# Performance work log

Measured on AMD Instinct MI355X. Metric: run time of the kernel, lower is better.

The kernel has to match this reference:

```python
import jax, jax.numpy as jnp
import numpy as np

EPS = 1e-5
S_CENTERS = 1024  # npoint//4
NSAMPLE = 32


def index_points(pts, idx):
    # pts [B,N,C], idx [B,...] int -> [B,...,C]
    return jax.vmap(lambda p, i: p[i])(pts, idx)


def farthest_point_sample(xyz, npoint):
    # xyz [B,N,3] -> [B,npoint] indices (deterministic start at index 0)
    B, N, _ = xyz.shape
    def body(carry, _):
        dist, far = carry
        centroid = jnp.take_along_axis(xyz, far[:, None, None], axis=1)  # [B,1,3]
        d = jnp.sum((xyz - centroid) ** 2, axis=-1)                      # [B,N]
        dist = jnp.minimum(dist, d)
        nxt = jnp.argmax(dist, axis=-1).astype(jnp.int32)
        return (dist, nxt), far
    init = (jnp.full((B, N), 1e10, xyz.dtype), jnp.zeros((B,), jnp.int32))
    _, idx = jax.lax.scan(body, init, None, length=npoint)
    return jnp.transpose(idx)  # [B,npoint]


def knn_point(k, xyz, new_xyz):
    # squared dists [B,S,N], take k nearest
    d = (jnp.sum(new_xyz ** 2, -1)[:, :, None]
         + jnp.sum(xyz ** 2, -1)[:, None, :]
         - 2.0 * jnp.einsum('bsc,bnc->bsn', new_xyz, xyz))
    _, idx = jax.lax.top_k(-d, k)
    return idx  # [B,S,k]


def instance_norm(h):
    # h [B,S,K,C]: InstanceNorm2d (affine=False) normalizes per (b,c) over spatial dims
    mu = jnp.mean(h, axis=(1, 2), keepdims=True)
    var = jnp.var(h, axis=(1, 2), keepdims=True)
    return (h - mu) * jax.lax.rsqrt(var + EPS)


def setup_inputs() -> dict:
    key = jax.random.key(0)
    ks = jax.random.split(key, 12)
    B, N, C = 8, 4096, 128
    inp = {
        'pc1_l_loc2': jax.random.normal(ks[0], (B, 3, N), jnp.float32),
        'corr_feats': jax.random.normal(ks[1], (B, C, N), jnp.float32),
        'W1': jax.random.normal(ks[2], (128, 131), jnp.float32) * 0.05,
        'b1': jnp.zeros((128,), jnp.float32),
        'W2': jax.random.normal(ks[3], (128, 128), jnp.float32) * 0.05,
        'b2': jnp.zeros((128,), jnp.float32),
        'W3': jax.random.normal(ks[4], (128, 128), jnp.float32) * 0.05,
        'b3': jnp.zeros((128,), jnp.float32),
        'fc_w': jax.random.normal(ks[5], (3, 128), jnp.float32) * 0.05,
        'fc_b': jnp.zeros((3,), jnp.float32),
    }
    return inp


def reference(pc1_l_loc2, corr_feats, W1, b1, W2, b2, W3, b3, fc_w, fc_b):
    xyz = jnp.transpose(pc1_l_loc2, (0, 2, 1))    # [B,N,3]
    points = jnp.transpose(corr_feats, (0, 2, 1))  # [B,N,128]

    fps_idx = farthest_point_sample(xyz, S_CENTERS)           # [B,S]
    new_xyz = index_points(xyz, fps_idx)                      # [B,S,3]
    idx = knn_point(NSAMPLE, xyz, new_xyz)                    # [B,S,K]
    grouped_xyz = index_points(xyz, idx)                      # [B,S,K,3]
    grouped_xyz_norm = grouped_xyz - new_xyz[:, :, None, :]
    grouped_pts = index_points(points, idx)                   # [B,S,K,128]
    h = jnp.concatenate([grouped_xyz_norm, grouped_pts], -1)  # [B,S,K,131]

    for W, b in ((W1, b1), (W2, b2), (W3, b3)):
        h = jnp.einsum('bskc,oc->bsko', h, W) + b  # 1x1 conv as matmul
        h = jax.nn.relu(instance_norm(h))

    x = jnp.max(h, axis=2)                         # [B,S,128] max over neighbors
    x = jnp.einsum('bsc,oc->bso', x, fc_w) + fc_b  # [B,S,3]
    flow0 = jnp.transpose(x, (0, 2, 1))            # [B,3,S]
    return flow0
```

## Files before the change

### kernel.cpp

```cpp
#include <hip/hip_runtime.h>
#include <hip/hip_fp16.h>

#define NB 8
#define NPTS 4096
#define NS 1024
#define NK 32
#define NM (NB*NS*NK)
#define NWORK 504

typedef _Float16 f16x8 __attribute__((ext_vector_type(8)));
typedef float    f32x4 __attribute__((ext_vector_type(4)));
typedef float    f32x2 __attribute__((ext_vector_type(2)));

__device__ __forceinline__ float bf2f(unsigned short u){ return __uint_as_float(((unsigned)u)<<16); }
__device__ __forceinline__ unsigned short f2bf(float f){
  unsigned u = __float_as_uint(f);
  u = u + 0x7fffu + ((u>>16)&1u);
  return (unsigned short)(u>>16);
}
__device__ __forceinline__ unsigned long long umax64(unsigned long long a, unsigned long long b){ return a>b?a:b; }

#define DPP_STEP_MAX(x, ctrl, rm) { \
  unsigned _t = (unsigned)__builtin_amdgcn_update_dpp((int)(x), (int)(x), (ctrl), (rm), 0xf, false); \
  (x) = ((x) > _t) ? (x) : _t; }

__device__ __forceinline__ unsigned wave_max_u32(unsigned x){
  DPP_STEP_MAX(x, 0x111, 0xf);
  DPP_STEP_MAX(x, 0x112, 0xf);
  DPP_STEP_MAX(x, 0x114, 0xf);
  DPP_STEP_MAX(x, 0x118, 0xf);
  DPP_STEP_MAX(x, 0x142, 0xa);
  DPP_STEP_MAX(x, 0x143, 0xc);
  return (unsigned)__builtin_amdgcn_readlane((int)x, 63);
}

__device__ __forceinline__ bool detect_f32(const unsigned short* __restrict__ u){
  int huge_=0, zero_=0;
  #pragma unroll
  for (int i=0;i<64;i++){
    unsigned short w = u[i];
    if ((w & 0x7fffu) == 0) { zero_++; continue; }
    float a = fabsf(bf2f(w));
    if (a > 1e6f || a < 1e-6f) huge_++;
  }
  return (huge_ >= 8) || (zero_ >= 24);
}
__device__ __forceinline__ float ldin(const void* p, size_t i, bool f32){
  if (f32) return ((const float*)p)[i];
  else     return bf2f(((const unsigned short*)p)[i]);
}

__global__ __launch_bounds__(256, 2) void fps_knn_fused(
    const void* __restrict__ pc1,
    const void* __restrict__ feats,
    int* __restrict__ fps_out,
    _Float16* __restrict__ G,
    float* __restrict__ statz,
    float* __restrict__ new_xyz,
    int* __restrict__ knn_idx)
{
  __shared__ __align__(16) char smem[65600];
  int t = threadIdx.x;
  const bool f32 = detect_f32((const unsigned short*)pc1);
  if (blockIdx.x < 8){
    __builtin_amdgcn_s_setprio(1);
    float4* cp4 = (float4*)smem;
    unsigned long long (*part)[4] = (unsigned long long (*)[4])(smem + 65536);
    int b = blockIdx.x;
    const size_t base = (size_t)b*3*NPTS;
    for (int i=t;i<NPTS;i+=256){
      float4 v;
      v.x = ldin(pc1, base+i, f32);
      v.y = ldin(pc1, base+NPTS+i, f32);
      v.z = ldin(pc1, base+2*NPTS+i, f32);
      v.w = 0.f;
      cp4[i] = v;
    }
    __syncthreads();
    f32x2 px[8],py[8],pz[8],dist[8];
    #pragma unroll
    for (int j=0;j<8;j++){
      float4 a = cp4[t*16+2*j], c = cp4[t*16+2*j+1];
      px[j] = f32x2{a.x, c.x};
      py[j] = f32x2{a.y, c.y};
      pz[j] = f32x2{a.z, c.z};
      dist[j] = f32x2{1e10f, 1e10f};
    }
    int far = 0;
    int w = t>>6, lane = t&63;
    for (int it=0; it<NS; it++){
      if (t==0)
        __hip_atomic_store(&fps_out[b*NS+it], far, __ATOMIC_RELAXED, __HIP_MEMORY_SCOPE_AGENT);
      float4 cc = cp4[far];
      f32x2 vcx = f32x2{cc.x,cc.x}, vcy = f32x2{cc.y,cc.y}, vcz = f32x2{cc.z,cc.z};
      {
        #pragma clang fp contract(off)
        #pragma unroll
        for (int j=0;j<8;j++){
          f32x2 dx = px[j]-vcx, dy = py[j]-vcy, dz = pz[j]-vcz;
          f32x2 d  = (dx*dx + dy*dy) + dz*dz;
          dist[j]  = __builtin_elementwise_min(dist[j], d);
        }
      }
      float d_[16];
      #pragma unroll
      for (int j=0;j<8;j++){ d_[2*j]=dist[j][0]; d_[2*j+1]=dist[j][1]; }
      float a0 = fmaxf(fmaxf(d_[0],d_[1]),d_[2]);
      float a1 = fmaxf(fmaxf(d_[3],d_[4]),d_[5]);
      float a2 = fmaxf(fmaxf(d_[6],d_[7]),d_[8]);
      float a3 = fmaxf(fmaxf(d_[9],d_[10]),d_[11]);
      float a4 = fmaxf(fmaxf(d_[12],d_[13]),d_[14]);
      float b0 = fmaxf(fmaxf(a0,a1),a2);
      float b1 = fmaxf(fmaxf(a3,a4),d_[15]);
      float bl = fmaxf(b0,b1);
      int li = 0;
      #pragma unroll
      for (int i=15;i>=0;i--) if (d_[i]==bl) li = i;
      unsigned blu = __float_as_uint(bl);
      unsigned wm = wave_max_u32(blu);
      unsigned long long mk = __ballot(blu == wm);
      int l = __builtin_ctzll(mk);
      int idx = __builtin_amdgcn_readlane(t*16+li, l);
      if (lane==0) part[it&1][w] = ((unsigned long long)wm<<32) | (unsigned)(NPTS-1-idx);
      asm volatile("s_waitcnt lgkmcnt(0)" ::: "memory");
      __builtin_amdgcn_s_barrier();
      __builtin_amdgcn_sched_barrier(0);
      const ulonglong2* pp = (const ulonglong2*)&part[it&1][0];
      ulonglong2 A = pp[0], B = pp[1];
      unsigned long long m = umax64(umax64(A.x,A.y), umax64(B.x,B.y));
      far = NPTS-1 - (int)(m & 0xffffffffu);
    }
  } else {
    int wid = blockIdx.x - 8;
    {
      float (*tile)[65] = (float (*)[65])smem;
      if (wid==0){
        for (int i=t;i<6144;i+=256) statz[i]=0.f;
      }
      for (int b2 = wid; b2 < 512; b2 += NWORK){
        int b = b2>>6, n0 = (b2&63)*64;
        #pragma unroll 4
        for (int i=0;i<32;i++){
          int idx = i*256 + t;
          int c = idx>>6, n = idx&63;
          tile[c][n] = ldin(feats, ((size_t)b*128 + c)*NPTS + n0 + n, f32);
        }
        __syncthreads();
        #pragma unroll 4
        for (int i=0;i<32;i++){
          int idx = i*256 + t;
          int n = idx>>7, c = idx&127;
          G[((size_t)b*NPTS + n0 + n)*136 + 3 + c] = (_Float16)tile[c][n];
        }
        if (t<64){
          size_t gb = ((size_t)b*NPTS + n0 + t)*136;
          G[gb]=(_Float16)0.f; G[gb+1]=(_Float16)0.f; G[gb+2]=(_Float16)0.f;
          #pragma unroll
          for (int c=131;c<136;c++) G[gb+c]=(_Float16)0.f;
        }
        __syncthreads();
      }
    }
    __syncthreads();
    unsigned* hist            = (unsigned*)smem;
    unsigned long long* cand  = (unsigned long long*)(smem + 16384);
    unsigned* partk           = (unsigned*)(smem + 20480);
    unsigned* sup             = (unsigned*)(smem + 21504);
    unsigned* scal            = (unsigned*)(smem + 21568);
    int* sn0                  = (int*)(smem + 21576);
    for (int ci = wid; ci < NB*NS; ci += NWORK){
      int b = ci & 7, s = ci >> 3;
      int blk = (b<<10) | s;
      if (t==0){
        int nv;
        while ((nv = __hip_atomic_load(&fps_out[b*NS+s], __ATOMIC_RELAXED,
                                       __HIP_MEMORY_SCOPE_AGENT)) == -1)
          __builtin_amdgcn_s_sleep(16);
        *sn0 = nv;
      }
      __syncthreads();
      const size_t base = (size_t)b*3*NPTS;
      int n0 = *sn0;
      float qx = ldin(pc1, base+n0, f32);
      float qy = ldin(pc1, base+NPTS+n0, f32);
      float qz = ldin(pc1, base+2*NPTS+n0, f32);
      if (t==0){
        new_xyz[(size_t)blk*3]=qx; new_xyz[(size_t)blk*3+1]=qy; new_xyz[(size_t)blk*3+2]=qz;
        scal[0]=0u;
      }
      #pragma unroll
      for (int j=0;j<16;j++) hist[j*256 + t] = 0u;
      float qn = __fadd_rn(__fadd_rn(__fmul_rn(qx,qx),__fmul_rn(qy,qy)),__fmul_rn(qz,qz));
      unsigned dv[16];
      #pragma unroll
      for (int k=0;k<16;k++){
        int n = t + 256*k;
        float x = ldin(pc1, base+n, f32);
        float y = ldin(pc1, base+NPTS+n, f32);
        float z = ldin(pc1, base+2*NPTS+n, f32);
        float pn = __fadd_rn(__fadd_rn(__fmul_rn(x,x),__fmul_rn(y,y)),__fmul_rn(z,z));
        float dt = __fadd_rn(__fadd_rn(__fmul_rn(qx,x),__fmul_rn(qy,y)),__fmul_rn(qz,z));
        float d  = __fsub_rn(__fadd_rn(qn,pn), __fmul_rn(2.f,dt));
        unsigned u = __float_as_uint(d);
        dv[k] = (u & 0x80000000u) ? ~u : (u | 0x80000000u);
      }
      __syncthreads();
      #pragma unroll
      for (int k=0;k<16;k++)
        atomicAdd(&hist[dv[k]>>20], 1u);
      __syncthreads();
      {
        unsigned ssum = 0;
        const uint4* hp = (const uint4*)&hist[t*16];
        #pragma unroll
        for (int j=0;j<4;j++){
          uint4 v = hp[j];
          ssum += v.x + v.y + v.z + v.w;
        }
        partk[t] = ssum;
      }
      __syncthreads();
      if (t < 16){
        unsigned qq = 0;
        #pragma unroll
        for (int j=0;j<16;j++) qq += partk[t*16 + j];
        sup[t] = qq;
      }
      __syncthreads();
      if (t == 0){
        unsigned acc = 0; int sb = 0;
        for (; sb < 16; sb++){ unsigned v = sup[sb]; if (acc + v >= NK) break; acc += v; }
        int pt = sb*16;
        for (; pt < sb*16+16; pt++){ unsigned v = partk[pt]; if (acc + v >= NK) break; acc += v; }
        int bn = pt*16;
        for (; bn < pt*16+16; bn++){ unsigned v = hist[bn]; if (acc + v >= NK) break; acc += v; }
        scal[1] = (unsigned)bn;
      }
      __syncthreads();
      unsigned beta = scal[1];
      #pragma unroll
      for (int k=0;k<16;k++){
        if ((dv[k]>>20) <= beta){
          unsigned pos = atomicAdd(&scal[0], 1u);
          if (pos < 512u)
            cand[pos] = ((unsigned long long)dv[k]<<32) | (unsigned)(t + 256*k);
        }
      }
      __syncthreads();
      int C = (int)scal[0]; if (C > 512) C = 512;
      for (int tt = t; tt < C; tt += 256){
        unsigned long long K = cand[tt];
        int rank = 0;
        for (int j = 0; j < C; j++) rank += (cand[j] < K) ? 1 : 0;
        if (rank < NK) knn_idx[(size_t)blk*NK + rank] = (int)(K & 0xffffffffu);
      }
      __syncthreads();
    }
  }
}

template<int LAYER>
__global__ __launch_bounds__(256)
__attribute__((amdgpu_waves_per_eu(1,3)))
void conv_mfma(
    const void* __restrict__ pc1,
    const _Float16* __restrict__ G,
    const int* __restrict__ knn_idx,
    const float* __restrict__ new_xyz,
    const _Float16* __restrict__ Hin,
    const float* __restrict__ gp1,
    const float* __restrict__ gp2,
    const void* __restrict__ W,
    _Float16* __restrict__ Hout,
    float* __restrict__ gs1, float* __restrict__ gs2)
{
  constexpr int KC  = (LAYER==1)?131:128;
  constexpr int KCP = (LAYER==1)?160:128;
  constexpr int HSW = (LAYER==1)?168:136;
  __shared__ __align__(16) _Float16 hs[128][HSW];
  __shared__ __align__(16) _Float16 wt[(LAYER==1)?128:1][40];
  __shared__ float red1[4][64], red2[4][64];
  __shared__ int   nidx[128];
  __shared__ float cxyz[4][3];
  __shared__ __align__(16) _Float16 smuh[128], srsh[128];
  int blk = blockIdx.x;
  int m0 = blk*128;
  int b  = m0 >> 15;
  int t  = threadIdx.x;
  const bool f32 = detect_f32((const unsigned short*)pc1);
  int w = t>>6, lane = t&63;
  int l16 = lane&15, q = lane>>4, q8 = q*8;
  int wr = (w&1)*64, wc = (w>>1)*64;

  if (LAYER==1){
    if (t<128) nidx[t] = knn_idx[m0+t];
    if (t<12)  cxyz[t/3][t%3] = new_xyz[(size_t)(m0>>5)*3 + t];
    __syncthreads();
    for (int u=t; u<128*17; u+=256){
      int p = u/17, qq = u - p*17;
      const f16x8* src = (const f16x8*)(G + ((size_t)b*NPTS + nidx[p])*136 + qq*8);
      *(f16x8*)&hs[p][qq*8] = *src;
    }
    for (int u=t; u<128*3; u+=256){
      int p = u/3, qq = u - p*3;
      uint4 z; z.x=z.y=z.z=z.w=0u;
      *(uint4*)&hs[p][136+qq*8] = z;
    }
    __syncthreads();
    if (t<128){
      int n = nidx[t];
      float cx = cxyz[t>>5][0], cy = cxyz[t>>5][1], cz = cxyz[t>>5][2];
      hs[t][0] = (_Float16)(ldin(pc1, ((size_t)b*3+0)*NPTS+n, f32) - cx);
      hs[t][1] = (_Float16)(ldin(pc1, ((size_t)b*3+1)*NPTS+n, f32) - cy);
      hs[t][2] = (_Float16)(ldin(pc1, ((size_t)b*3+2)*NPTS+n, f32) - cz);
    }
    __syncthreads();
  } else {
    if (t<128){
      const float inv = 1.0f/32768.0f;
      float m = gp1[b*128+t]*inv;
      smuh[t] = (_Float16)m;
      srsh[t] = (_Float16)rsqrtf(gp2[b*128+t]*inv - m*m + 1e-5f);
    }
    __syncthreads();
    int p = t & 127, hi = t>>7;
    const _Float16* src = Hin + (size_t)(m0+p)*128 + hi*64;
    f16x8 zero8 = {};
    #pragma unroll
    for (int j=0;j<8;j++){
      f16x8 v   = *(const f16x8*)(src + j*8);
      f16x8 mu8 = *(const f16x8*)&smuh[hi*64 + j*8];
      f16x8 rs8 = *(const f16x8*)&srsh[hi*64 + j*8];
      f16x8 o = (v - mu8) * rs8;
      o = __builtin_elementwise_max(o, zero8);
      *(f16x8*)&hs[p][hi*64 + j*8] = o;
    }
    __syncthreads();
  }

  f32x4 acc[4][4];
  #pragma unroll
  for (int i=0;i<4;i++)
    #pragma unroll
    for (int c=0;c<4;c++){ acc[i][c][0]=0.f; acc[i][c][1]=0.f; acc[i][c][2]=0.f; acc[i][c][3]=0.f; }

  if (LAYER==1){
    for (int k0=0; k0<KCP; k0+=32){
      {
        int o = t>>1, half = t&1;
        f16x8 w0, w1;
        #pragma unroll
        for (int jj=0;jj<8;jj++){
          int c0 = k0 + half*16 + jj, c1 = c0 + 8;
          w0[jj] = (_Float16)((c0<KC) ? ldin(W, (size_t)o*KC + c0, f32) : 0.f);
          w1[jj] = (_Float16)((c1<KC) ? ldin(W, (size_t)o*KC + c1, f32) : 0.f);
        }
        *(f16x8*)&wt[o][half*16]     = w0;
        *(f16x8*)&wt[o][half*16 + 8] = w1;
      }
      __syncthreads();
      f16x8 av[4], bv[4];
      #pragma unroll
      for (int i=0;i<4;i++) av[i] = *(const f16x8*)&hs[wr + i*16 + l16][k0 + q8];
      #pragma unroll
      for (int c=0;c<4;c++) bv[c] = *(const f16x8*)&wt[wc + c*16 + l16][q8];
      #pragma unroll
      for (int i=0;i<4;i++)
        #pragma unroll
        for (int c=0;c<4;c++)
          acc[i][c] = __builtin_amdgcn_mfma_f32_16x16x32_f16(av[i], bv[c], acc[i][c], 0,0,0);
      __syncthreads();
    }
  } else {
    #pragma unroll
    for (int k0=0; k0<128; k0+=32){
      f16x8 av[4], bv[4];
      #pragma unroll
      for (int i=0;i<4;i++) av[i] = *(const f16x8*)&hs[wr + i*16 + l16][k0 + q8];
      #pragma unroll
      for (int c=0;c<4;c++){
        int row = wc + c*16 + l16;
        if (f32){
          const f32x4* Wr = (const f32x4*)((const float*)W + (size_t)row*128 + k0 + q8);
          f32x4 v0 = Wr[0], v1 = Wr[1];
          f16x8 bb;
          bb[0]=(_Float16)v0[0]; bb[1]=(_Float16)v0[1]; bb[2]=(_Float16)v0[2]; bb[3]=(_Float16)v0[3];
          bb[4]=(_Float16)v1[0]; bb[5]=(_Float16)v1[1]; bb[6]=(_Float16)v1[2]; bb[7]=(_Float16)v1[3];
          bv[c] = bb;
        } else {
          const ushort4* Wr = (const ushort4*)((const unsigned short*)W + (size_t)row*128 + k0 + q8);
          ushort4 u0 = Wr[0], u1 = Wr[1];
          f16x8 bb;
          bb[0]=(_Float16)bf2f(u0.x); bb[1]=(_Float16)bf2f(u0.y); bb[2]=(_Float16)bf2f(u0.z); bb[3]=(_Float16)bf2f(u0.w);
          bb[4]=(_Float16)bf2f(u1.x); bb[5]=(_Float16)bf2f(u1.y); bb[6]=(_Float16)bf2f(u1.z); bb[7]=(_Float16)bf2f(u1.w);
          bv[c] = bb;
        }
      }
      #pragma unroll
      for (int i=0;i<4;i++)
        #pragma unroll
        for (int c=0;c<4;c++)
          acc[i][c] = __builtin_amdgcn_mfma_f32_16x16x32_f16(av[i], bv[c], acc[i][c], 0,0,0);
    }
    __syncthreads();
  }

  #pragma unroll
  for (int c=0;c<4;c++){
    int o = wc + c*16 + l16;
    float s1=0.f, s2=0.f;
    #pragma unroll
    for (int i=0;i<4;i++){
      int row = wr + i*16 + q*4;
      #pragma unroll
      for (int r=0;r<4;r++){
        float v = acc[i][c][r];
        hs[row + r][o] = (_Float16)v;
        s1 += v; s2 = fmaf(v,v,s2);
      }
    }
    s1 += __shfl_xor(s1, 16, 64); s1 += __shfl_xor(s1, 32, 64);
    s2 += __shfl_xor(s2, 16, 64); s2 += __shfl_xor(s2, 32, 64);
    if (q==0){ red1[w][c*16+l16] = s1; red2[w][c*16+l16] = s2; }
  }
  __syncthreads();
  _Float16* dst0 = Hout + (size_t)m0*128;
  #pragma unroll
  for (int j=0;j<8;j++){
    int fi = j*256 + t;
    int row = fi >> 4, col = (fi & 15)*8;
    *(f16x8*)(dst0 + (size_t)fi*8) = *(const f16x8*)&hs[row][col];
  }
  if (t<128){
    int lo = t & 63, g = (t>>6)*2;
    unsafeAtomicAdd(&gs1[b*128+t], red1[g][lo] + red1[g+1][lo]);
    unsafeAtomicAdd(&gs2[b*128+t], red2[g][lo] + red2[g+1][lo]);
  }
}

__global__ __launch_bounds__(128) void final_kernel(
    const void* __restrict__ pc1,
    const _Float16* __restrict__ H,
    const float* __restrict__ gp1, const float* __restrict__ gp2,
    const void* __restrict__ fc_w, const void* __restrict__ fc_b,
    void* __restrict__ outv)
{
  __shared__ __align__(16) _Float16 tile[32][136];
  __shared__ float mv[128];
  int blk = blockIdx.x;
  int b = blk>>10, s = blk & 1023;
  int o = threadIdx.x;
  const bool f32 = detect_f32((const unsigned short*)pc1);
  const _Float16* src = H + (size_t)blk*NK*128;
  #pragma unroll
  for (int j=0;j<4;j++){
    int fi = j*128 + o;
    int row = fi >> 4, col = (fi & 15)*8;
    *(f16x8*)&tile[row][col] = *(const f16x8*)(src + (size_t)fi*8);
  }
  __syncthreads();
  int bo = b*128 + o;
  const float inv = 1.0f/32768.0f;
  float mu_ = gp1[bo]*inv;
  float rs_ = rsqrtf(gp2[bo]*inv - mu_*mu_ + 1e-5f);
  float m = -1e30f;
  #pragma unroll 4
  for (int k=0;k<NK;k++){
    float v = ((float)tile[k][o] - mu_)*rs_;
    m = fmaxf(m, v);
  }
  m = fmaxf(m, 0.f);
  mv[o] = m;
  __syncthreads();
  if (o<3){
    float acc = ldin(fc_b, o, f32);
    for(int c=0;c<128;c++) acc = fmaf(ldin(fc_w, (size_t)o*128+c, f32), mv[c], acc);
    size_t oi = ((size_t)b*3 + o)*NS + s;
    if (f32) ((float*)outv)[oi] = acc;
    else     ((unsigned short*)outv)[oi] = f2bf(acc);
  }
}

extern "C" void kernel_launch(void* const* d_in, const int* in_sizes, int n_in,
                              void* d_out, int out_size, void* d_ws, size_t ws_size,
                              hipStream_t stream){
  const void* pc1   = d_in[0];
  const void* feats = d_in[1];
  const void* W1    = d_in[2];
  const void* W2    = d_in[4];
  const void* W3    = d_in[6];
  const void* fcw   = d_in[8];
  const void* fcb   = d_in[9];
  char* ws = (char*)d_ws;
  int*      fps  = (int*)     (ws + 0);
  float*    nxyz = (float*)   (ws + 32768);
  int*      knn  = (int*)     (ws + 131072);
  float*    st   = (float*)   (ws + 1179648);
  _Float16* Ha   = (_Float16*)(ws + 1204224);
  _Float16* Hb   = (_Float16*)(ws + 68313088);
  _Float16* G    = Hb;

  (void)hipMemsetAsync(fps, 0xFF, NB*NS*sizeof(int), stream);

  fps_knn_fused<<<8 + NWORK, 256, 0, stream>>>(pc1, feats, fps, G, st, nxyz, knn);

  conv_mfma<1><<<NM/128, 256, 0, stream>>>(pc1, G, knn, nxyz,
      (const _Float16*)nullptr, (const float*)nullptr, (const float*)nullptr,
      W1, Ha, st, st+1024);
  conv_mfma<2><<<NM/128, 256, 0, stream>>>(pc1, G, knn, nxyz,
      Ha, st, st+1024, W2, Hb, st+2048, st+3072);
  conv_mfma<3><<<NM/128, 256, 0, stream>>>(pc1, G, knn, nxyz,
      Hb, st+2048, st+3072, W3, Ha, st+4096, st+5120);

  final_kernel<<<NB*NS, 128, 0, stream>>>(pc1, Ha, st+4096, st+5120, fcw, fcb, d_out);
}
```

Before: 954.8 us.

## Fuse neighbor max-pool into layer-3 GEMM epilogue and simplify FPS barrier

The layer-3 GEMM epilogue now reduces each group of 32 neighbor rows to a per-channel max in shared memory and writes only that, instead of storing the full activation tensor. The final kernel then reads one value per channel and applies the instance norm and ReLU to the max. This is valid only because normalization with a positive scale preserves ordering. The goal is to remove most of the layer-3 write and re-read traffic. The FPS loop also replaces a hand-rolled waitcnt, barrier and sched_barrier sequence with __syncthreads, which may change scheduling in that hot serial loop.

```diff
diff --git a/kernel.cpp b/kernel.cpp
--- a/kernel.cpp
+++ b/kernel.cpp
@@ -122,9 +122,7 @@
       int l = __builtin_ctzll(mk);
       int idx = __builtin_amdgcn_readlane(t*16+li, l);
       if (lane==0) part[it&1][w] = ((unsigned long long)wm<<32) | (unsigned)(NPTS-1-idx);
-      asm volatile("s_waitcnt lgkmcnt(0)" ::: "memory");
-      __builtin_amdgcn_s_barrier();
-      __builtin_amdgcn_sched_barrier(0);
+      __syncthreads();
       const ulonglong2* pp = (const ulonglong2*)&part[it&1][0];
       ulonglong2 A = pp[0], B = pp[1];
       unsigned long long m = umax64(umax64(A.x,A.y), umax64(B.x,B.y));
@@ -424,12 +422,27 @@
     if (q==0){ red1[w][c*16+l16] = s1; red2[w][c*16+l16] = s2; }
   }
   __syncthreads();
-  _Float16* dst0 = Hout + (size_t)m0*128;
-  #pragma unroll
-  for (int j=0;j<8;j++){
-    int fi = j*256 + t;
-    int row = fi >> 4, col = (fi & 15)*8;
-    *(f16x8*)(dst0 + (size_t)fi*8) = *(const f16x8*)&hs[row][col];
+  if (LAYER==3){
+    if (t<128){
+      #pragma unroll
+      for (int c4=0;c4<4;c4++){
+        _Float16 mx = hs[c4*32][t];
+        #pragma unroll
+        for (int r=1;r<32;r++){
+          _Float16 v = hs[c4*32 + r][t];
+          mx = (v > mx) ? v : mx;
+        }
+        Hout[(size_t)(blk*4 + c4)*128 + t] = mx;
+      }
+    }
+  } else {
+    _Float16* dst0 = Hout + (size_t)m0*128;
+    #pragma unroll
+    for (int j=0;j<8;j++){
+      int fi = j*256 + t;
+      int row = fi >> 4, col = (fi & 15)*8;
+      *(f16x8*)(dst0 + (size_t)fi*8) = *(const f16x8*)&hs[row][col];
+    }
   }
   if (t<128){
     int lo = t & 63, g = (t>>6)*2;
@@ -440,37 +453,23 @@
 
 __global__ __launch_bounds__(128) void final_kernel(
     const void* __restrict__ pc1,
-    const _Float16* __restrict__ H,
+    const _Float16* __restrict__ M,
     const float* __restrict__ gp1, const float* __restrict__ gp2,
     const void* __restrict__ fc_w, const void* __restrict__ fc_b,
     void* __restrict__ outv)
 {
-  __shared__ __align__(16) _Float16 tile[32][136];
   __shared__ float mv[128];
   int blk = blockIdx.x;
   int b = blk>>10, s = blk & 1023;
   int o = threadIdx.x;
   const bool f32 = detect_f32((const unsigned short*)pc1);
-  const _Float16* src = H + (size_t)blk*NK*128;
-  #pragma unroll
-  for (int j=0;j<4;j++){
-    int fi = j*128 + o;
-    int row = fi >> 4, col = (fi & 15)*8;
-    *(f16x8*)&tile[row][col] = *(const f16x8*)(src + (size_t)fi*8);
-  }
-  __syncthreads();
+  float mraw = (float)M[(size_t)blk*128 + o];
   int bo = b*128 + o;
   const float inv = 1.0f/32768.0f;
   float mu_ = gp1[bo]*inv;
   float rs_ = rsqrtf(gp2[bo]*inv - mu_*mu_ + 1e-5f);
-  float m = -1e30f;
-  #pragma unroll 4
-  for (int k=0;k<NK;k++){
-    float v = ((float)tile[k][o] - mu_)*rs_;
-    m = fmaxf(m, v);
-  }
-  m = fmaxf(m, 0.f);
-  mv[o] = m;
+  float v = fmaxf((mraw - mu_)*rs_, 0.f);
+  mv[o] = v;
   __syncthreads();
   if (o<3){
     float acc = ldin(fc_b, o, f32);
```

Result: no change. 943.4 us (-1.2%).
